# Performance work log

Measured on AMD Instinct MI355X. Metric: run time of the kernel, lower is better.

The kernel has to match this reference:

```python
import jax, jax.numpy as jnp
import numpy as np

B, S, T, DIM, H, W, HEADS = 4, 16, 16, 512, 32, 32, 8


def setup_inputs() -> dict:
    key = jax.random.key(0)
    ks = jax.random.split(key, 6)
    q = jax.random.normal(ks[0], (B, S, DIM, H, W), dtype=jnp.float32)
    k = jax.random.normal(ks[1], (B, T, DIM, H, W), dtype=jnp.float32)
    v = jax.random.normal(ks[2], (B, T, DIM, H, W), dtype=jnp.float32)
    Wq = jax.random.normal(ks[3], (DIM, DIM), dtype=jnp.float32) * (DIM ** -0.5)
    Wk = jax.random.normal(ks[4], (DIM, DIM), dtype=jnp.float32) * (DIM ** -0.5)
    Wv = jax.random.normal(ks[5], (DIM, DIM), dtype=jnp.float32) * (DIM ** -0.5)
    return {"q": q, "k": k, "v": v, "Wq": Wq, "Wk": Wk, "Wv": Wv, "heads": HEADS}


def reference(q, k, v, Wq, Wk, Wv, heads):
    b, s, d, h, w = q.shape
    t = k.shape[1]
    dh = d // heads
    scale = dh ** -0.5
    # pooled Q/K: spatial mean then linear (nn.Linear: x @ W.T)
    qm = jnp.mean(q, axis=(-1, -2)) @ Wq.T            # [B,S,D]
    km = jnp.mean(k, axis=(-1, -2)) @ Wk.T            # [B,T,D]
    # per-pixel V: permute(0,-1,-2,1,2) -> [B,W,H,T,D], flatten W*H (W-major, as torch)
    vp = jnp.transpose(v, (0, 4, 3, 1, 2)).reshape(b, w * h, t, d) @ Wv.T  # [B,HW,T,D]
    qh = qm.reshape(b, s, heads, dh) * scale          # [B,S,h,dh]
    kh = km.reshape(b, t, heads, dh)                  # [B,T,h,dh]
    vh = vp.reshape(b, w * h, t, heads, dh)           # [B,HW,T,h,dh]
    attn = jax.nn.softmax(jnp.einsum('bshd,bthd->bhst', qh, kh), axis=-1)  # [B,h,S,T]
    out = jnp.einsum('bhst,bpthd->bpshd', attn, vh)   # [B,HW,S,h,dh]
    # torch: out [B,HW,h,S,dh].permute(0,3,2,4,1) -> [B,S,h,dh,HW] -> view(B,S,D,H,W)
    out = jnp.transpose(out, (0, 2, 3, 4, 1)).reshape(b, s, d, h, w)
    return out
```

## Files before the change

### kernel.cpp

```cpp
#include <hip/hip_runtime.h>


__device__ __forceinline__ unsigned short f2bf(float f) {
  union { float f; unsigned int u; } x; x.f = f;
  unsigned int r = x.u + 0x7fffu + ((x.u >> 16) & 1u);
  return (unsigned short)(r >> 16);
}

typedef __attribute__((ext_vector_type(8))) __bf16 bf16x8;
typedef __attribute__((ext_vector_type(4))) float f32x4;

__global__ __launch_bounds__(256) void k_means(const float* __restrict__ q,
                                               const float* __restrict__ k,
                                               float* __restrict__ qm,
                                               float* __restrict__ km) {
  int n = blockIdx.x;
  const float* src = (n < 8192) ? q : k;
  float* dst = (n < 8192) ? qm : km;
  int chan = (n & 8191) * 4 + (threadIdx.x >> 6);
  int lane = threadIdx.x & 63;
  const float4* p = (const float4*)(src + (size_t)chan * 1024);
  float s = 0.f;
#pragma unroll
  for (int i = 0; i < 4; ++i) {
    float4 f = p[i * 64 + lane];
    s += f.x + f.y + f.z + f.w;
  }
#pragma unroll
  for (int off = 32; off > 0; off >>= 1) s += __shfl_down(s, off);
  if (lane == 0) dst[chan] = s * (1.0f / 1024.0f);
}

__global__ __launch_bounds__(256) void k_trans(const float* __restrict__ v,
                                               unsigned short* __restrict__ vT) {
  int tid = threadIdx.x;
  int m0 = blockIdx.x * 64, c0 = blockIdx.y * 64, bt = blockIdx.z;
  __shared__ float ls[64 * 65];
  const float* src = v + (size_t)bt * 524288;
#pragma unroll
  for (int p = 0; p < 4; ++p) {
    int r = p * 16 + (tid >> 4);
    int mm4 = (tid & 15) * 4;
    float4 f = *(const float4*)&src[(size_t)(c0 + r) * 1024 + m0 + mm4];
    ls[r * 65 + mm4 + 0] = f.x;
    ls[r * 65 + mm4 + 1] = f.y;
    ls[r * 65 + mm4 + 2] = f.z;
    ls[r * 65 + mm4 + 3] = f.w;
  }
  __syncthreads();
  unsigned short* dst = vT + (size_t)bt * 524288;
#pragma unroll
  for (int p = 0; p < 2; ++p) {
    int mm = p * 32 + (tid >> 3);
    int cr8 = (tid & 7) * 8;
    unsigned int w[4];
#pragma unroll
    for (int e = 0; e < 4; ++e) {
      unsigned short lo = f2bf(ls[(cr8 + 2 * e + 0) * 65 + mm]);
      unsigned short hi = f2bf(ls[(cr8 + 2 * e + 1) * 65 + mm]);
      w[e] = (unsigned int)lo | ((unsigned int)hi << 16);
    }
    uint4 pk = {w[0], w[1], w[2], w[3]};
    int x = m0 + mm;
    int rr = ((x & 31) << 5) | (x >> 5);
    *(uint4*)&dst[(size_t)rr * 512 + c0 + cr8] = pk;
  }
}

__global__ __launch_bounds__(256) void k_attn(const float* __restrict__ qm,
                                              const float* __restrict__ km,
                                              const float* __restrict__ Wq,
                                              const float* __restrict__ Wk,
                                              const float* __restrict__ Wv,
                                              unsigned short* __restrict__ Wv_bf,
                                              float* __restrict__ attnT) {
  int tid = threadIdx.x;
  int b = blockIdx.x >> 3, h = blockIdx.x & 7;
  {
    const float4* s4 = (const float4*)Wv;
#pragma unroll
    for (int i = 0; i < 8; ++i) {
      int idx = blockIdx.x * 256 + tid + i * 8192;
      float4 f = s4[idx];
      ushort4 u;
      u.x = f2bf(f.x); u.y = f2bf(f.y); u.z = f2bf(f.z); u.w = f2bf(f.w);
      *(ushort4*)&Wv_bf[(size_t)idx * 4] = u;
    }
  }
  __shared__ float WS[64 * 65];
  __shared__ float xS[16 * 64];
  __shared__ float qhS[16 * 65];
  __shared__ float khS[16 * 65];
  __shared__ float lg[16 * 17];
  int j = tid & 63, so = tid >> 6;
  float acc[4];

  acc[0] = acc[1] = acc[2] = acc[3] = 0.f;
  for (int c0 = 0; c0 < 512; c0 += 64) {
    __syncthreads();
#pragma unroll
    for (int p = 0; p < 4; ++p) {
      int r = p * 16 + (tid >> 4);
      int c4 = (tid & 15) * 4;
      float4 f = *(const float4*)&Wq[(size_t)(h * 64 + r) * 512 + c0 + c4];
      WS[r * 65 + c4 + 0] = f.x; WS[r * 65 + c4 + 1] = f.y;
      WS[r * 65 + c4 + 2] = f.z; WS[r * 65 + c4 + 3] = f.w;
    }
    {
      int s = tid >> 4;
      int c4 = (tid & 15) * 4;
      float4 f = *(const float4*)&qm[(size_t)(b * 16 + s) * 512 + c0 + c4];
      xS[s * 64 + c4 + 0] = f.x; xS[s * 64 + c4 + 1] = f.y;
      xS[s * 64 + c4 + 2] = f.z; xS[s * 64 + c4 + 3] = f.w;
    }
    __syncthreads();
    for (int cc = 0; cc < 64; ++cc) {
      float wv = WS[j * 65 + cc];
#pragma unroll
      for (int o = 0; o < 4; ++o) acc[o] += xS[(o * 4 + so) * 64 + cc] * wv;
    }
  }
#pragma unroll
  for (int o = 0; o < 4; ++o) qhS[(o * 4 + so) * 65 + j] = acc[o] * 0.125f;

  acc[0] = acc[1] = acc[2] = acc[3] = 0.f;
  for (int c0 = 0; c0 < 512; c0 += 64) {
    __syncthreads();
#pragma unroll
    for (int p = 0; p < 4; ++p) {
      int r = p * 16 + (tid >> 4);
      int c4 = (tid & 15) * 4;
      float4 f = *(const float4*)&Wk[(size_t)(h * 64 + r) * 512 + c0 + c4];
      WS[r * 65 + c4 + 0] = f.x; WS[r * 65 + c4 + 1] = f.y;
      WS[r * 65 + c4 + 2] = f.z; WS[r * 65 + c4 + 3] = f.w;
    }
    {
      int s = tid >> 4;
      int c4 = (tid & 15) * 4;
      float4 f = *(const float4*)&km[(size_t)(b * 16 + s) * 512 + c0 + c4];
      xS[s * 64 + c4 + 0] = f.x; xS[s * 64 + c4 + 1] = f.y;
      xS[s * 64 + c4 + 2] = f.z; xS[s * 64 + c4 + 3] = f.w;
    }
    __syncthreads();
    for (int cc = 0; cc < 64; ++cc) {
      float wv = WS[j * 65 + cc];
#pragma unroll
      for (int o = 0; o < 4; ++o) acc[o] += xS[(o * 4 + so) * 64 + cc] * wv;
    }
  }
#pragma unroll
  for (int o = 0; o < 4; ++o) khS[(o * 4 + so) * 65 + j] = acc[o];
  __syncthreads();

  {
    int s = tid >> 4, t = tid & 15;
    float a = 0.f;
    for (int jj = 0; jj < 64; ++jj) a += qhS[s * 65 + jj] * khS[t * 65 + jj];
    lg[s * 17 + t] = a;
  }
  __syncthreads();
  if (tid < 16) {
    int s = tid;
    float mx = -1e30f;
#pragma unroll
    for (int t = 0; t < 16; ++t) mx = fmaxf(mx, lg[s * 17 + t]);
    float e[16], sum = 0.f;
#pragma unroll
    for (int t = 0; t < 16; ++t) { e[t] = __expf(lg[s * 17 + t] - mx); sum += e[t]; }
    float inv = 1.0f / sum;
#pragma unroll
    for (int t = 0; t < 16; ++t)
      attnT[(blockIdx.x) * 256 + t * 16 + s] = e[t] * inv;
  }
}

__global__ __launch_bounds__(256) void k_gemm(const unsigned short* __restrict__ Wv_bf,
                                              const unsigned short* __restrict__ vT,
                                              float* __restrict__ VP) {
  int tid = threadIdx.x;
  int bx = blockIdx.x, by = blockIdx.y, bz = blockIdx.z;
  __shared__ __align__(16) unsigned short As[128 * 32];
  __shared__ __align__(16) unsigned short Bs[128 * 32];
  const unsigned short* Ag = Wv_bf + (size_t)(by * 128) * 512;
  const unsigned short* Bg = vT + (size_t)bz * 524288 + (size_t)(bx * 128) * 512;
  int r = tid >> 2;
  int c8 = (tid & 3) * 8;
  int lane = tid & 63, wave = tid >> 6;
  int wd = wave >> 1, wm = wave & 1;
  int l15 = lane & 15, quad = lane >> 4;

  f32x4 acc[4][4];
#pragma unroll
  for (int i = 0; i < 4; ++i)
#pragma unroll
    for (int j = 0; j < 4; ++j) acc[i][j] = (f32x4){0.f, 0.f, 0.f, 0.f};

  for (int kk = 0; kk < 16; ++kk) {
    int c0 = kk * 32;
    if (kk) __syncthreads();
    __builtin_amdgcn_global_load_lds(
        (const __attribute__((address_space(1))) void*)(Ag + (size_t)r * 512 + c0 + c8),
        (__attribute__((address_space(3))) void*)&As[tid * 8], 16, 0, 0);
    __builtin_amdgcn_global_load_lds(
        (const __attribute__((address_space(1))) void*)(Ag + (size_t)(r + 64) * 512 + c0 + c8),
        (__attribute__((address_space(3))) void*)&As[2048 + tid * 8], 16, 0, 0);
    __builtin_amdgcn_global_load_lds(
        (const __attribute__((address_space(1))) void*)(Bg + (size_t)r * 512 + c0 + c8),
        (__attribute__((address_space(3))) void*)&Bs[tid * 8], 16, 0, 0);
    __builtin_amdgcn_global_load_lds(
        (const __attribute__((address_space(1))) void*)(Bg + (size_t)(r + 64) * 512 + c0 + c8),
        (__attribute__((address_space(3))) void*)&Bs[2048 + tid * 8], 16, 0, 0);
    __syncthreads();

    bf16x8 af[4], bfr[4];
#pragma unroll
    for (int i = 0; i < 4; ++i)
      af[i] = *(const bf16x8*)&As[(wd * 64 + i * 16 + l15) * 32 + quad * 8];
#pragma unroll
    for (int j = 0; j < 4; ++j)
      bfr[j] = *(const bf16x8*)&Bs[(wm * 64 + j * 16 + l15) * 32 + quad * 8];
#pragma unroll
    for (int i = 0; i < 4; ++i)
#pragma unroll
      for (int j = 0; j < 4; ++j)
        acc[i][j] = __builtin_amdgcn_mfma_f32_16x16x32_bf16(af[i], bfr[j], acc[i][j], 0, 0, 0);
  }

  float* outp = VP + (size_t)bz * 524288;
#pragma unroll
  for (int i = 0; i < 4; ++i) {
#pragma unroll
    for (int j = 0; j < 4; ++j) {
      int m = bx * 128 + wm * 64 + j * 16 + l15;
#pragma unroll
      for (int rr = 0; rr < 4; ++rr) {
        int d = by * 128 + wd * 64 + i * 16 + quad * 4 + rr;
        outp[(size_t)d * 1024 + m] = acc[i][j][rr];
      }
    }
  }
}

__global__ __launch_bounds__(256) void k_mix(float* __restrict__ out,
                                             const float* __restrict__ attnT) {
  int blk = blockIdx.x;
  int b = blk >> 9, d = blk & 511, h = d >> 6;
  int tid = threadIdx.x;
  const float* at = attnT + (b * 8 + h) * 256;
  size_t base = ((size_t)(b * 16) * 512 + d) * 1024 + tid * 4;

  float res[16][4];
#pragma unroll
  for (int s = 0; s < 16; ++s)
#pragma unroll
    for (int j = 0; j < 4; ++j) res[s][j] = 0.f;

#pragma unroll
  for (int t = 0; t < 16; ++t) {
    float4 vp = *(const float4*)&out[base + (size_t)t * 524288];
#pragma unroll
    for (int s = 0; s < 16; ++s) {
      float a = at[t * 16 + s];
      res[s][0] += a * vp.x; res[s][1] += a * vp.y;
      res[s][2] += a * vp.z; res[s][3] += a * vp.w;
    }
  }

#pragma unroll
  for (int s = 0; s < 16; ++s) {
    float4 f = {res[s][0], res[s][1], res[s][2], res[s][3]};
    *(float4*)&out[base + (size_t)s * 524288] = f;
  }
}

extern "C" void kernel_launch(void* const* d_in, const int* in_sizes, int n_in,
                              void* d_out, int out_size, void* d_ws, size_t ws_size,
                              hipStream_t stream) {
  const float* q  = (const float*)d_in[0];
  const float* k  = (const float*)d_in[1];
  const float* v  = (const float*)d_in[2];
  const float* Wq = (const float*)d_in[3];
  const float* Wk = (const float*)d_in[4];
  const float* Wv = (const float*)d_in[5];

  char* ws = (char*)d_ws;
  unsigned short* vT    = (unsigned short*)ws;
  unsigned short* Wv_bf = (unsigned short*)(ws + 67108864);
  float* qm    = (float*)(ws + 67633152);
  float* km    = (float*)(ws + 67764224);
  float* attnT = (float*)(ws + 67895296);
  float* out   = (float*)d_out;

  k_means<<<16384, 256, 0, stream>>>(q, k, qm, km);
  k_trans<<<dim3(16, 8, 64), 256, 0, stream>>>(v, vT);
  k_attn<<<32, 256, 0, stream>>>(qm, km, Wq, Wk, Wv, Wv_bf, attnT);
  k_gemm<<<dim3(8, 4, 64), 256, 0, stream>>>(Wv_bf, vT, out);
  k_mix<<<2048, 256, 0, stream>>>(out, attnT);
}
```

Measured before the change: 535.1 us.

## Switch GEMM operands to fp16 and store projected V as fp16 intermediate

Changes the V projection GEMM from bf16 to fp16 MFMA inputs. When workspace allows, it writes the projected V to a separate fp16 buffer, and a new mix kernel reads it, halving intermediate write and read traffic compared with going through the fp32 output buffer. The means kernel now makes each wave reduce eight channels, and the transpose kernel loops over four batch slices per block, which cuts the number of blocks launched. fp16 range and precision differ from bf16, and the fp16 path only runs if the workspace is large enough.

```diff
diff --git a/kernel.cpp b/kernel.cpp
--- a/kernel.cpp
+++ b/kernel.cpp
@@ -1,69 +1,85 @@
 #include <hip/hip_runtime.h>
 
 
-__device__ __forceinline__ unsigned short f2bf(float f) {
-  union { float f; unsigned int u; } x; x.f = f;
-  unsigned int r = x.u + 0x7fffu + ((x.u >> 16) & 1u);
-  return (unsigned short)(r >> 16);
-}
-
-typedef __attribute__((ext_vector_type(8))) __bf16 bf16x8;
+typedef __attribute__((ext_vector_type(8))) _Float16 f16x8;
+typedef __attribute__((ext_vector_type(4))) _Float16 f16x4;
 typedef __attribute__((ext_vector_type(4))) float f32x4;
+
+__device__ __forceinline__ unsigned short f2h(float f) {
+  union { _Float16 h; unsigned short u; } x;
+  x.h = (_Float16)f;
+  return x.u;
+}
 
 __global__ __launch_bounds__(256) void k_means(const float* __restrict__ q,
                                                const float* __restrict__ k,
                                                float* __restrict__ qm,
                                                float* __restrict__ km) {
-  int n = blockIdx.x;
-  const float* src = (n < 8192) ? q : k;
-  float* dst = (n < 8192) ? qm : km;
-  int chan = (n & 8191) * 4 + (threadIdx.x >> 6);
+  int gw = blockIdx.x * 4 + (threadIdx.x >> 6);
   int lane = threadIdx.x & 63;
-  const float4* p = (const float4*)(src + (size_t)chan * 1024);
-  float s = 0.f;
-#pragma unroll
-  for (int i = 0; i < 4; ++i) {
-    float4 f = p[i * 64 + lane];
-    s += f.x + f.y + f.z + f.w;
-  }
-#pragma unroll
-  for (int off = 32; off > 0; off >>= 1) s += __shfl_down(s, off);
-  if (lane == 0) dst[chan] = s * (1.0f / 1024.0f);
+  int ch0 = gw * 8;
+  const float* src = q; float* dst = qm; int base = ch0;
+  if (ch0 >= 32768) { src = k; dst = km; base = ch0 - 32768; }
+  const float4* p = (const float4*)src;
+#pragma unroll
+  for (int j = 0; j < 8; j += 2) {
+    const float4* p0 = p + (size_t)(base + j) * 256;
+    const float4* p1 = p0 + 256;
+    float4 a0 = p0[lane], a1 = p0[64 + lane], a2 = p0[128 + lane], a3 = p0[192 + lane];
+    float4 b0 = p1[lane], b1 = p1[64 + lane], b2 = p1[128 + lane], b3 = p1[192 + lane];
+    float s0 = (a0.x + a0.y + a0.z + a0.w) + (a1.x + a1.y + a1.z + a1.w) +
+               (a2.x + a2.y + a2.z + a2.w) + (a3.x + a3.y + a3.z + a3.w);
+    float s1 = (b0.x + b0.y + b0.z + b0.w) + (b1.x + b1.y + b1.z + b1.w) +
+               (b2.x + b2.y + b2.z + b2.w) + (b3.x + b3.y + b3.z + b3.w);
+#pragma unroll
+    for (int off = 32; off > 0; off >>= 1) {
+      s0 += __shfl_down(s0, off);
+      s1 += __shfl_down(s1, off);
+    }
+    if (lane == 0) {
+      dst[base + j]     = s0 * (1.0f / 1024.0f);
+      dst[base + j + 1] = s1 * (1.0f / 1024.0f);
+    }
+  }
 }
 
 __global__ __launch_bounds__(256) void k_trans(const float* __restrict__ v,
                                                unsigned short* __restrict__ vT) {
   int tid = threadIdx.x;
-  int m0 = blockIdx.x * 64, c0 = blockIdx.y * 64, bt = blockIdx.z;
+  int m0 = blockIdx.x * 64, c0 = blockIdx.y * 64;
   __shared__ float ls[64 * 65];
-  const float* src = v + (size_t)bt * 524288;
-#pragma unroll
-  for (int p = 0; p < 4; ++p) {
-    int r = p * 16 + (tid >> 4);
-    int mm4 = (tid & 15) * 4;
-    float4 f = *(const float4*)&src[(size_t)(c0 + r) * 1024 + m0 + mm4];
-    ls[r * 65 + mm4 + 0] = f.x;
-    ls[r * 65 + mm4 + 1] = f.y;
-    ls[r * 65 + mm4 + 2] = f.z;
-    ls[r * 65 + mm4 + 3] = f.w;
-  }
-  __syncthreads();
-  unsigned short* dst = vT + (size_t)bt * 524288;
-#pragma unroll
-  for (int p = 0; p < 2; ++p) {
-    int mm = p * 32 + (tid >> 3);
-    int cr8 = (tid & 7) * 8;
-    unsigned int w[4];
-#pragma unroll
-    for (int e = 0; e < 4; ++e) {
-      unsigned short lo = f2bf(ls[(cr8 + 2 * e + 0) * 65 + mm]);
-      unsigned short hi = f2bf(ls[(cr8 + 2 * e + 1) * 65 + mm]);
-      w[e] = (unsigned int)lo | ((unsigned int)hi << 16);
-    }
-    uint4 pk = {w[0], w[1], w[2], w[3]};
-    int x = m0 + mm;
-    int rr = ((x & 31) << 5) | (x >> 5);
-    *(uint4*)&dst[(size_t)rr * 512 + c0 + cr8] = pk;
+  for (int it = 0; it < 4; ++it) {
+    int bt = blockIdx.z * 4 + it;
+    const float* src = v + (size_t)bt * 524288;
+    if (it) __syncthreads();
+#pragma unroll
+    for (int p = 0; p < 4; ++p) {
+      int r = p * 16 + (tid >> 4);
+      int mm4 = (tid & 15) * 4;
+      float4 f = *(const float4*)&src[(size_t)(c0 + r) * 1024 + m0 + mm4];
+      ls[r * 65 + mm4 + 0] = f.x;
+      ls[r * 65 + mm4 + 1] = f.y;
+      ls[r * 65 + mm4 + 2] = f.z;
+      ls[r * 65 + mm4 + 3] = f.w;
+    }
+    __syncthreads();
+    unsigned short* dst = vT + (size_t)bt * 524288;
+#pragma unroll
+    for (int p = 0; p < 2; ++p) {
+      int mm = p * 32 + (tid >> 3);
+      int cr8 = (tid & 7) * 8;
+      unsigned int w[4];
+#pragma unroll
+      for (int e = 0; e < 4; ++e) {
+        unsigned short lo = f2h(ls[(cr8 + 2 * e + 0) * 65 + mm]);
+        unsigned short hi = f2h(ls[(cr8 + 2 * e + 1) * 65 + mm]);
+        w[e] = (unsigned int)lo | ((unsigned int)hi << 16);
+      }
+      uint4 pk = {w[0], w[1], w[2], w[3]};
+      int x = m0 + mm;
+      int rr = ((x & 31) << 5) | (x >> 5);
+      *(uint4*)&dst[(size_t)rr * 512 + c0 + cr8] = pk;
+    }
   }
 }
 
@@ -72,7 +88,7 @@
                                               const float* __restrict__ Wq,
                                               const float* __restrict__ Wk,
                                               const float* __restrict__ Wv,
-                                              unsigned short* __restrict__ Wv_bf,
+                                              unsigned short* __restrict__ Wv_h,
                                               float* __restrict__ attnT) {
   int tid = threadIdx.x;
   int b = blockIdx.x >> 3, h = blockIdx.x & 7;
@@ -83,8 +99,8 @@
       int idx = blockIdx.x * 256 + tid + i * 8192;
       float4 f = s4[idx];
       ushort4 u;
-      u.x = f2bf(f.x); u.y = f2bf(f.y); u.z = f2bf(f.z); u.w = f2bf(f.w);
-      *(ushort4*)&Wv_bf[(size_t)idx * 4] = u;
+      u.x = f2h(f.x); u.y = f2h(f.y); u.z = f2h(f.z); u.w = f2h(f.w);
+      *(ushort4*)&Wv_h[(size_t)idx * 4] = u;
     }
   }
   __shared__ float WS[64 * 65];
@@ -174,14 +190,14 @@
   }
 }
 
-__global__ __launch_bounds__(256) void k_gemm(const unsigned short* __restrict__ Wv_bf,
+__global__ __launch_bounds__(256) void k_gemm(const unsigned short* __restrict__ Wv_h,
                                               const unsigned short* __restrict__ vT,
-                                              float* __restrict__ VP) {
+                                              void* __restrict__ VP, int f16out) {
   int tid = threadIdx.x;
   int bx = blockIdx.x, by = blockIdx.y, bz = blockIdx.z;
   __shared__ __align__(16) unsigned short As[128 * 32];
   __shared__ __align__(16) unsigned short Bs[128 * 32];
-  const unsigned short* Ag = Wv_bf + (size_t)(by * 128) * 512;
+  const unsigned short* Ag = Wv_h + (size_t)(by * 128) * 512;
   const unsigned short* Bg = vT + (size_t)bz * 524288 + (size_t)(bx * 128) * 512;
   int r = tid >> 2;
   int c8 = (tid & 3) * 8;
@@ -212,32 +228,80 @@
         (__attribute__((address_space(3))) void*)&Bs[2048 + tid * 8], 16, 0, 0);
     __syncthreads();
 
-    bf16x8 af[4], bfr[4];
+    f16x8 af[4], bfr[4];
 #pragma unroll
     for (int i = 0; i < 4; ++i)
-      af[i] = *(const bf16x8*)&As[(wd * 64 + i * 16 + l15) * 32 + quad * 8];
+      af[i] = *(const f16x8*)&As[(wd * 64 + i * 16 + l15) * 32 + quad * 8];
 #pragma unroll
     for (int j = 0; j < 4; ++j)
-      bfr[j] = *(const bf16x8*)&Bs[(wm * 64 + j * 16 + l15) * 32 + quad * 8];
+      bfr[j] = *(const f16x8*)&Bs[(wm * 64 + j * 16 + l15) * 32 + quad * 8];
 #pragma unroll
     for (int i = 0; i < 4; ++i)
 #pragma unroll
       for (int j = 0; j < 4; ++j)
-        acc[i][j] = __builtin_amdgcn_mfma_f32_16x16x32_bf16(af[i], bfr[j], acc[i][j], 0, 0, 0);
-  }
-
-  float* outp = VP + (size_t)bz * 524288;
-#pragma unroll
-  for (int i = 0; i < 4; ++i) {
-#pragma unroll
-    for (int j = 0; j < 4; ++j) {
-      int m = bx * 128 + wm * 64 + j * 16 + l15;
-#pragma unroll
-      for (int rr = 0; rr < 4; ++rr) {
-        int d = by * 128 + wd * 64 + i * 16 + quad * 4 + rr;
-        outp[(size_t)d * 1024 + m] = acc[i][j][rr];
+        acc[i][j] = __builtin_amdgcn_mfma_f32_16x16x32_f16(af[i], bfr[j], acc[i][j], 0, 0, 0);
+  }
+
+  if (f16out) {
+    _Float16* outp = (_Float16*)VP + (size_t)bz * 524288;
+#pragma unroll
+    for (int i = 0; i < 4; ++i)
+#pragma unroll
+      for (int j = 0; j < 4; ++j) {
+        int m = bx * 128 + wm * 64 + j * 16 + l15;
+#pragma unroll
+        for (int rr = 0; rr < 4; ++rr) {
+          int d = by * 128 + wd * 64 + i * 16 + quad * 4 + rr;
+          outp[(size_t)d * 1024 + m] = (_Float16)acc[i][j][rr];
+        }
       }
-    }
+  } else {
+    float* outp = (float*)VP + (size_t)bz * 524288;
+#pragma unroll
+    for (int i = 0; i < 4; ++i)
+#pragma unroll
+      for (int j = 0; j < 4; ++j) {
+        int m = bx * 128 + wm * 64 + j * 16 + l15;
+#pragma unroll
+        for (int rr = 0; rr < 4; ++rr) {
+          int d = by * 128 + wd * 64 + i * 16 + quad * 4 + rr;
+          outp[(size_t)d * 1024 + m] = acc[i][j][rr];
+        }
+      }
+  }
+}
+
+__global__ __launch_bounds__(256) void k_mix_f16(const _Float16* __restrict__ VP,
+                                                 float* __restrict__ out,
+                                                 const float* __restrict__ attnT) {
+  int blk = blockIdx.x;
+  int b = blk >> 9, d = blk & 511, h = d >> 6;
+  int tid = threadIdx.x;
+  const float* at = attnT + (b * 8 + h) * 256;
+  size_t base = ((size_t)(b * 16) * 512 + d) * 1024 + tid * 4;
+
+  float res[16][4];
+#pragma unroll
+  for (int s = 0; s < 16; ++s)
+#pragma unroll
+    for (int j = 0; j < 4; ++j) res[s][j] = 0.f;
+
+#pragma unroll
+  for (int t = 0; t < 16; ++t) {
+    f16x4 vp = *(const f16x4*)&VP[base + (size_t)t * 524288];
+    float x0 = (float)vp[0], x1 = (float)vp[1], x2 = (float)vp[2], x3 = (float)vp[3];
+#pragma unroll
+    for (int s = 0; s < 16; ++s) {
+      float a = at[t * 16 + s];
+      res[s][0] += a * x0; res[s][1] += a * x1;
+      res[s][2] += a * x2; res[s][3] += a * x3;
+    }
+  }
+
+#pragma unroll
+  for (int s = 0; s < 16; ++s) {
+    float4 f = {res[s][0], res[s][1], res[s][2], res[s][3]};
+    *(float4*)&out[base + (size_t)s * 524288] = f;
   }
 }
 
@@ -285,15 +349,24 @@
 
   char* ws = (char*)d_ws;
   unsigned short* vT    = (unsigned short*)ws;
-  unsigned short* Wv_bf = (unsigned short*)(ws + 67108864);
+  unsigned short* Wv_h  = (unsigned short*)(ws + 67108864);
   float* qm    = (float*)(ws + 67633152);
   float* km    = (float*)(ws + 67764224);
   float* attnT = (float*)(ws + 67895296);
+  _Float16* VPh = (_Float16*)(ws + 67928064);
   float* out   = (float*)d_out;
 
-  k_means<<<16384, 256, 0, stream>>>(q, k, qm, km);
-  k_trans<<<dim3(16, 8, 64), 256, 0, stream>>>(v, vT);
-  k_attn<<<32, 256, 0, stream>>>(qm, km, Wq, Wk, Wv, Wv_bf, attnT);
-  k_gemm<<<dim3(8, 4, 64), 256, 0, stream>>>(Wv_bf, vT, out);
-  k_mix<<<2048, 256, 0, stream>>>(out, attnT);
-}
+  const size_t NEED_F16 = 67928064ull + 67108864ull;
+  int use16 = (ws_size >= NEED_F16) ? 1 : 0;
+
+  k_means<<<2048, 256, 0, stream>>>(q, k, qm, km);
+  k_trans<<<dim3(16, 8, 16), 256, 0, stream>>>(v, vT);
+  k_attn<<<32, 256, 0, stream>>>(qm, km, Wq, Wk, Wv, Wv_h, attnT);
+  if (use16) {
+    k_gemm<<<dim3(8, 4, 64), 256, 0, stream>>>(Wv_h, vT, (void*)VPh, 1);
+    k_mix_f16<<<2048, 256, 0, stream>>>(VPh, out, attnT);
+  } else {
+    k_gemm<<<dim3(8, 4, 64), 256, 0, stream>>>(Wv_h, vT, (void*)out, 0);
+    k_mix<<<2048, 256, 0, stream>>>(out, attnT);
+  }
+}
```

Measured after the change: 550.1 us. 2.8% more time.
